# Optimization experiments

Hardware: AMD Instinct MI355X
Metric: run time of the kernel (lower is better)

Reference implementation:

```python
import jax, jax.numpy as jnp
import numpy as np

N = 100000      # nodes
E = 1600000     # edges
D_IN = 16       # input_dim
D_H = 32        # hidden_dim
D_OUT = 1       # output_dim
N_ITERS = 2
D_CAT = D_H + D_IN          # node feature after cat([H, X])
D_EDGE = 2 * D_CAT          # edge MLP input dim


def setup_inputs() -> dict:
    key = jax.random.key(0)
    ks = jax.random.split(key, 10)
    x = jax.random.normal(ks[0], (N, D_IN), jnp.float32)
    edge_index = jax.random.randint(ks[1], (2, E), 0, N, dtype=jnp.int32)
    # inputnet: Linear(D_IN -> D_H) + Tanh
    W_in = jax.random.normal(ks[2], (D_H, D_IN), jnp.float32) / np.sqrt(D_IN)
    b_in = jnp.zeros((D_H,), jnp.float32)
    # convnn (EdgeConv nn): Linear(D_EDGE -> D_H) + Sigmoid
    W_c = jax.random.normal(ks[3], (D_H, D_EDGE), jnp.float32) / np.sqrt(D_EDGE)
    b_c = jnp.zeros((D_H,), jnp.float32)
    # outputnet: Linear(D_H -> D_OUT) + Sigmoid
    W_out = jax.random.normal(ks[4], (D_OUT, D_H), jnp.float32) / np.sqrt(D_H)
    b_out = jnp.zeros((D_OUT,), jnp.float32)
    return {"x": x, "edge_index": edge_index, "W_in": W_in, "b_in": b_in,
            "W_c": W_c, "b_c": b_c, "W_out": W_out, "b_out": b_out}


def reference(x, edge_index, W_in, b_in, W_c, b_c, W_out, b_out):
    src = edge_index[0]  # x_j (source / neighbor)
    dst = edge_index[1]  # x_i (target, aggregation index)

    H = jnp.tanh(x @ W_in.T + b_in)            # [N, D_H]
    feats = jnp.concatenate([H, x], axis=-1)    # [N, D_CAT]

    for _ in range(N_ITERS):
        xi = feats[dst]                          # [E, D_CAT] gather targets
        xj = feats[src]                          # [E, D_CAT] gather sources
        # PyG EdgeConv message: nn(cat([x_i, x_j - x_i]))
        msg = jax.nn.sigmoid(
            jnp.concatenate([xi, xj - xi], axis=-1) @ W_c.T + b_c)  # [E, D_H]
        H = jax.ops.segment_sum(msg, dst, num_segments=N)           # aggr='add'
        feats = jnp.concatenate([H, x], axis=-1)

    sum_H = jnp.mean(H, axis=0)                  # [D_H]
    return jax.nn.sigmoid(sum_H @ W_out.T + b_out)  # [D_OUT]
```

## Files before the change

kernel.cpp:

```cpp
#include <hip/hip_runtime.h>

#define D_H 32
#define NREP 32
#define SLOTS 48
#define BIN_SHIFT 8
#define MAXNB 512
#define BIN_CAP 5120
#define SB 256
#define PNPB 64
#define SF 52

__device__ __forceinline__ float sigf(float v) {
    return 1.f / (1.f + __expf(-v));
}


__global__ __launch_bounds__(256) void k_ab0(const float* __restrict__ x,
                      const float* __restrict__ W_in, const float* __restrict__ b_in,
                      const float* __restrict__ W_c, const float* __restrict__ b_c,
                      float* __restrict__ A, float* __restrict__ B, int N) {
    __shared__ float f[PNPB][SF];
    int tid = threadIdx.x;
    int n0 = blockIdx.x * PNPB;
    int wv = tid >> 6;
    int h  = (tid >> 5) & 1;
    int j  = tid & 31;
    float wc[96];
    {
        const float4* wr = (const float4*)(W_c + j * 96);
#pragma unroll
        for (int q = 0; q < 24; ++q) {
            float4 v = wr[q];
            wc[4 * q] = v.x; wc[4 * q + 1] = v.y; wc[4 * q + 2] = v.z; wc[4 * q + 3] = v.w;
        }
    }
    float win[16];
    {
        const float4* wr = (const float4*)(W_in + j * 16);
#pragma unroll
        for (int q = 0; q < 4; ++q) {
            float4 v = wr[q];
            win[4 * q] = v.x; win[4 * q + 1] = v.y; win[4 * q + 2] = v.z; win[4 * q + 3] = v.w;
        }
    }
    float bc = b_c[j];
    float bi = b_in[j];
    {
        int row = tid >> 2, c = tid & 3;
        float4 v = {0.f, 0.f, 0.f, 0.f};
        if (n0 + row < N) v = ((const float4*)(x + (size_t)(n0 + row) * 16))[c];
        *(float4*)&f[row][32 + 4 * c] = v;
    }
    __syncthreads();
#pragma unroll 2
    for (int it = 0; it < 8; ++it) {
        int n = wv * 16 + it * 2 + h;
        {
            float4 x0 = *(const float4*)&f[n][32];
            float4 x1 = *(const float4*)&f[n][36];
            float4 x2 = *(const float4*)&f[n][40];
            float4 x3 = *(const float4*)&f[n][44];
            float acc = bi;
            acc += x0.x * win[0] + x0.y * win[1] + x0.z * win[2] + x0.w * win[3];
            acc += x1.x * win[4] + x1.y * win[5] + x1.z * win[6] + x1.w * win[7];
            acc += x2.x * win[8] + x2.y * win[9] + x2.z * win[10] + x2.w * win[11];
            acc += x3.x * win[12] + x3.y * win[13] + x3.z * win[14] + x3.w * win[15];
            f[n][j] = tanhf(acc);
        }
        float p = bc, bb = 0.f;
#pragma unroll
        for (int q = 0; q < 12; ++q) {
            float4 v = *(const float4*)&f[n][4 * q];
            p  += v.x * wc[4 * q]      + v.y * wc[4 * q + 1]
                + v.z * wc[4 * q + 2]  + v.w * wc[4 * q + 3];
            bb += v.x * wc[48 + 4 * q]     + v.y * wc[48 + 4 * q + 1]
                + v.z * wc[48 + 4 * q + 2] + v.w * wc[48 + 4 * q + 3];
        }
        int g = n0 + n;
        if (g < N) {
            A[(size_t)g * D_H + j] = p - bb;
            B[(size_t)g * D_H + j] = bb;
        }
    }
}

__global__ __launch_bounds__(256) void k_ab1(const float* __restrict__ H,
                      const float* __restrict__ x, const float* __restrict__ W_c,
                      const float* __restrict__ b_c, float* __restrict__ A,
                      float* __restrict__ B, int N) {
    __shared__ float f[PNPB][SF];
    int tid = threadIdx.x;
    int n0 = blockIdx.x * PNPB;
    int wv = tid >> 6;
    int h  = (tid >> 5) & 1;
    int j  = tid & 31;
    float wc[96];
    {
        const float4* wr = (const float4*)(W_c + j * 96);
#pragma unroll
        for (int q = 0; q < 24; ++q) {
            float4 v = wr[q];
            wc[4 * q] = v.x; wc[4 * q + 1] = v.y; wc[4 * q + 2] = v.z; wc[4 * q + 3] = v.w;
        }
    }
    float bc = b_c[j];
#pragma unroll
    for (int k = 0; k < 2; ++k) {
        int i = k * 256 + tid;
        int row = i >> 3, c = i & 7;
        float4 v = {0.f, 0.f, 0.f, 0.f};
        if (n0 + row < N) v = ((const float4*)(H + (size_t)(n0 + row) * D_H))[c];
        *(float4*)&f[row][4 * c] = v;
    }
    {
        int row = tid >> 2, c = tid & 3;
        float4 v = {0.f, 0.f, 0.f, 0.f};
        if (n0 + row < N) v = ((const float4*)(x + (size_t)(n0 + row) * 16))[c];
        *(float4*)&f[row][32 + 4 * c] = v;
    }
    __syncthreads();
#pragma unroll 2
    for (int it = 0; it < 8; ++it) {
        int n = wv * 16 + it * 2 + h;
        float p = bc, bb = 0.f;
#pragma unroll
        for (int q = 0; q < 12; ++q) {
            float4 v = *(const float4*)&f[n][4 * q];
            p  += v.x * wc[4 * q]      + v.y * wc[4 * q + 1]
                + v.z * wc[4 * q + 2]  + v.w * wc[4 * q + 3];
            bb += v.x * wc[48 + 4 * q]     + v.y * wc[48 + 4 * q + 1]
                + v.z * wc[48 + 4 * q + 2] + v.w * wc[48 + 4 * q + 3];
        }
        int g = n0 + n;
        if (g < N) {
            A[(size_t)g * D_H + j] = p - bb;
            B[(size_t)g * D_H + j] = bb;
        }
    }
}

__global__ __launch_bounds__(256) void k_bin(const int* __restrict__ src,
                                             const int* __restrict__ dst,
                                             int* __restrict__ binCnt,
                                             unsigned int* __restrict__ ebuf, int E) {
    __shared__ int hist[MAXNB];
    int tid = threadIdx.x;
    for (int i = tid; i < MAXNB; i += 256) hist[i] = 0;
    __syncthreads();
    int chunk = (E + SB - 1) / SB;
    int lo = blockIdx.x * chunk;
    int hi = lo + chunk; if (hi > E) hi = E;
    for (int e = lo + tid; e < hi; e += 256) {
        int b = dst[e] >> BIN_SHIFT;
        atomicAdd(&hist[b], 1);
    }
    __syncthreads();
    for (int b = tid; b < MAXNB; b += 256) {
        int c = hist[b];
        int base = c ? atomicAdd(&binCnt[b], c) : 0;
        hist[b] = b * BIN_CAP + base;
    }
    __syncthreads();
    for (int e = lo + tid; e < hi; e += 256) {
        int d = dst[e];
        int s = src[e];
        int b = d >> BIN_SHIFT;
        int pos = atomicAdd(&hist[b], 1);
        if ((unsigned)(pos - b * BIN_CAP) < (unsigned)BIN_CAP)
            ebuf[pos] = ((unsigned)(d & 255) << 24) | (unsigned)s;
    }
}

__global__ __launch_bounds__(256) void k_place(const int* __restrict__ binCnt,
                                               const unsigned int* __restrict__ ebuf,
                                               int* __restrict__ ssrcp,
                                               int* __restrict__ cntG,
                                               float* __restrict__ Srep, int N) {
    __shared__ int cnt[256];
    int tid = threadIdx.x;
    int w = blockIdx.x;
    if (w == 0) {
        float4 z = {0.f, 0.f, 0.f, 0.f};
        ((float4*)Srep)[tid];
        ((float4*)Srep)[tid] = z;
    }
    cnt[tid] = 0;
    __syncthreads();
    int n = binCnt[w]; if (n > BIN_CAP) n = BIN_CAP;
    int base = w * BIN_CAP;
    for (int j = tid; j < n; j += 256) {
        unsigned int v = ebuf[base + j];
        int ld = v >> 24;
        int s = v & 0xFFFFFF;
        int slot = atomicAdd(&cnt[ld], 1);
        if (slot < SLOTS)
            ssrcp[(size_t)((w << BIN_SHIFT) + ld) * SLOTS + slot] = s;
    }
    __syncthreads();
    int node = (w << BIN_SHIFT) + tid;
    if (node < N) cntG[node] = cnt[tid] < SLOTS ? cnt[tid] : SLOTS;
}


__global__ __launch_bounds__(256) void k_gather1(const int* __restrict__ cntG,
                          const int* __restrict__ ssrcp,
                          const float* __restrict__ A, const float* __restrict__ B,
                          float* __restrict__ H, int N) {
    int t = blockIdx.x * blockDim.x + threadIdx.x;
    int d = t >> 5;
    if (d >= N) return;
    int l = t & 31;
    int q = l & 7;
    int s = l >> 3;
    int len = cntG[d];
    const int* base = ssrcp + (size_t)d * SLOTS;
    float4 a4 = ((const float4*)(A + (size_t)d * D_H))[q];
    float4 acc = {0.f, 0.f, 0.f, 0.f};
    int j = s;
    for (; j + 12 < len; j += 16) {
        int i0 = base[j], i1 = base[j + 4], i2 = base[j + 8], i3 = base[j + 12];
        float4 b0 = ((const float4*)(B + (size_t)i0 * D_H))[q];
        float4 b1 = ((const float4*)(B + (size_t)i1 * D_H))[q];
        float4 b2 = ((const float4*)(B + (size_t)i2 * D_H))[q];
        float4 b3 = ((const float4*)(B + (size_t)i3 * D_H))[q];
        acc.x += sigf(a4.x + b0.x); acc.y += sigf(a4.y + b0.y);
        acc.z += sigf(a4.z + b0.z); acc.w += sigf(a4.w + b0.w);
        acc.x += sigf(a4.x + b1.x); acc.y += sigf(a4.y + b1.y);
        acc.z += sigf(a4.z + b1.z); acc.w += sigf(a4.w + b1.w);
        acc.x += sigf(a4.x + b2.x); acc.y += sigf(a4.y + b2.y);
        acc.z += sigf(a4.z + b2.z); acc.w += sigf(a4.w + b2.w);
        acc.x += sigf(a4.x + b3.x); acc.y += sigf(a4.y + b3.y);
        acc.z += sigf(a4.z + b3.z); acc.w += sigf(a4.w + b3.w);
    }
    for (; j + 4 < len; j += 8) {
        int i0 = base[j], i1 = base[j + 4];
        float4 b0 = ((const float4*)(B + (size_t)i0 * D_H))[q];
        float4 b1 = ((const float4*)(B + (size_t)i1 * D_H))[q];
        acc.x += sigf(a4.x + b0.x); acc.y += sigf(a4.y + b0.y);
        acc.z += sigf(a4.z + b0.z); acc.w += sigf(a4.w + b0.w);
        acc.x += sigf(a4.x + b1.x); acc.y += sigf(a4.y + b1.y);
        acc.z += sigf(a4.z + b1.z); acc.w += sigf(a4.w + b1.w);
    }
    if (j < len) {
        int i0 = base[j];
        float4 b0 = ((const float4*)(B + (size_t)i0 * D_H))[q];
        acc.x += sigf(a4.x + b0.x); acc.y += sigf(a4.y + b0.y);
        acc.z += sigf(a4.z + b0.z); acc.w += sigf(a4.w + b0.w);
    }
    acc.x += __shfl_xor(acc.x, 8);  acc.y += __shfl_xor(acc.y, 8);
    acc.z += __shfl_xor(acc.z, 8);  acc.w += __shfl_xor(acc.w, 8);
    acc.x += __shfl_xor(acc.x, 16); acc.y += __shfl_xor(acc.y, 16);
    acc.z += __shfl_xor(acc.z, 16); acc.w += __shfl_xor(acc.w, 16);
    if (s == 0) ((float4*)(H + (size_t)d * D_H))[q] = acc;
}

__global__ __launch_bounds__(256) void k_gather2(const int* __restrict__ cntG,
                          const int* __restrict__ ssrcp,
                          const float* __restrict__ A, const float* __restrict__ B,
                          float* __restrict__ Srep, int N) {
    int l = threadIdx.x & 31;
    int slot = threadIdx.x >> 5;
    int q = l & 7;
    int s = l >> 3;
    int d = blockIdx.x * 8 + slot;
    float4 acc = {0.f, 0.f, 0.f, 0.f};
    if (d < N) {
        int len = cntG[d];
        const int* base = ssrcp + (size_t)d * SLOTS;
        float4 a4 = ((const float4*)(A + (size_t)d * D_H))[q];
        int j = s;
        for (; j + 12 < len; j += 16) {
            int i0 = base[j], i1 = base[j + 4], i2 = base[j + 8], i3 = base[j + 12];
            float4 b0 = ((const float4*)(B + (size_t)i0 * D_H))[q];
            float4 b1 = ((const float4*)(B + (size_t)i1 * D_H))[q];
            float4 b2 = ((const float4*)(B + (size_t)i2 * D_H))[q];
            float4 b3 = ((const float4*)(B + (size_t)i3 * D_H))[q];
            acc.x += sigf(a4.x + b0.x); acc.y += sigf(a4.y + b0.y);
            acc.z += sigf(a4.z + b0.z); acc.w += sigf(a4.w + b0.w);
            acc.x += sigf(a4.x + b1.x); acc.y += sigf(a4.y + b1.y);
            acc.z += sigf(a4.z + b1.z); acc.w += sigf(a4.w + b1.w);
            acc.x += sigf(a4.x + b2.x); acc.y += sigf(a4.y + b2.y);
            acc.z += sigf(a4.z + b2.z); acc.w += sigf(a4.w + b2.w);
            acc.x += sigf(a4.x + b3.x); acc.y += sigf(a4.y + b3.y);
            acc.z += sigf(a4.z + b3.z); acc.w += sigf(a4.w + b3.w);
        }
        for (; j + 4 < len; j += 8) {
            int i0 = base[j], i1 = base[j + 4];
            float4 b0 = ((const float4*)(B + (size_t)i0 * D_H))[q];
            float4 b1 = ((const float4*)(B + (size_t)i1 * D_H))[q];
            acc.x += sigf(a4.x + b0.x); acc.y += sigf(a4.y + b0.y);
            acc.z += sigf(a4.z + b0.z); acc.w += sigf(a4.w + b0.w);
            acc.x += sigf(a4.x + b1.x); acc.y += sigf(a4.y + b1.y);
            acc.z += sigf(a4.z + b1.z); acc.w += sigf(a4.w + b1.w);
        }
        if (j < len) {
            int i0 = base[j];
            float4 b0 = ((const float4*)(B + (size_t)i0 * D_H))[q];
            acc.x += sigf(a4.x + b0.x); acc.y += sigf(a4.y + b0.y);
            acc.z += sigf(a4.z + b0.z); acc.w += sigf(a4.w + b0.w);
        }
    }
    acc.x += __shfl_xor(acc.x, 8);  acc.y += __shfl_xor(acc.y, 8);
    acc.z += __shfl_xor(acc.z, 8);  acc.w += __shfl_xor(acc.w, 8);
    acc.x += __shfl_xor(acc.x, 16); acc.y += __shfl_xor(acc.y, 16);
    acc.z += __shfl_xor(acc.z, 16); acc.w += __shfl_xor(acc.w, 16);
    __shared__ float red[8][32];
    if (s == 0) {
        red[slot][4 * q + 0] = acc.x;
        red[slot][4 * q + 1] = acc.y;
        red[slot][4 * q + 2] = acc.z;
        red[slot][4 * q + 3] = acc.w;
    }
    __syncthreads();
    if (threadIdx.x < 32) {
        float sm = 0.f;
#pragma unroll
        for (int r = 0; r < 8; ++r) sm += red[r][threadIdx.x];
        unsafeAtomicAdd(&Srep[(blockIdx.x & (NREP - 1)) * D_H + threadIdx.x], sm);
    }
}

__global__ void k_final(const float* __restrict__ Srep, const float* __restrict__ W_out,
                        const float* __restrict__ b_out, float* __restrict__ out,
                        float invN) {
    int j = threadIdx.x;
    float v = 0.f;
    if (j < 32) {
        float s = 0.f;
#pragma unroll
        for (int r = 0; r < NREP; ++r) s += Srep[r * D_H + j];
        v = s * invN * W_out[j];
    }
#pragma unroll
    for (int off = 32; off > 0; off >>= 1) v += __shfl_down(v, off);
    if (j == 0) out[0] = 1.f / (1.f + __expf(-(v + b_out[0])));
}

extern "C" void kernel_launch(void* const* d_in, const int* in_sizes, int n_in,
                              void* d_out, int out_size, void* d_ws, size_t ws_size,
                              hipStream_t stream) {
    const float* x     = (const float*)d_in[0];
    const int*   ei    = (const int*)d_in[1];
    const float* W_in  = (const float*)d_in[2];
    const float* b_in  = (const float*)d_in[3];
    const float* W_c   = (const float*)d_in[4];
    const float* b_c   = (const float*)d_in[5];
    const float* W_out = (const float*)d_in[6];
    const float* b_out = (const float*)d_in[7];

    const int N = in_sizes[0] / 16;
    const int E = in_sizes[1] / 2;
    const int* src = ei;
    const int* dst = ei + E;

    const int NB = (N + 255) >> BIN_SHIFT;

    float* H    = (float*)d_ws;
    float* A    = H + (size_t)N * D_H;
    float* B    = A + (size_t)N * D_H;
    float* Srep = B + (size_t)N * D_H;
    int*   cntG   = (int*)(Srep + NREP * D_H);
    int*   binCnt = cntG + N;
    int*   ssrcp  = binCnt + MAXNB;
    unsigned int* ebuf = (unsigned int*)H;

    float* out = (float*)d_out;

    const int abBlocks = (N + PNPB - 1) / PNPB;

    hipMemsetAsync(binCnt, 0, MAXNB * sizeof(int), stream);
    k_bin<<<SB, 256, 0, stream>>>(src, dst, binCnt, ebuf, E);
    k_place<<<NB, 256, 0, stream>>>(binCnt, ebuf, ssrcp, cntG, Srep, N);

    k_ab0<<<abBlocks, 256, 0, stream>>>(x, W_in, b_in, W_c, b_c, A, B, N);
    k_gather1<<<(int)(((size_t)N * 32 + 255) / 256), 256, 0, stream>>>(cntG, ssrcp, A, B, H, N);

    k_ab1<<<abBlocks, 256, 0, stream>>>(H, x, W_c, b_c, A, B, N);
    k_gather2<<<(N + 7) / 8, 256, 0, stream>>>(cntG, ssrcp, A, B, Srep, N);

    k_final<<<1, 64, 0, stream>>>(Srep, W_out, b_out, out, 1.f / (float)N);
}
```

Before: 267.4 us.

## Store gathered B in fp16, fold log2e scaling, vectorize neighbor index loads

The per-source B table is now stored as half precision and pre-scaled by -log2(e), and A is pre-scaled the same way. The gather loops can then compute the sigmoid with exp2 plus a hardware reciprocal, and each random neighbor fetch moves 8 bytes instead of 16. Neighbor lists are padded with zeros to a multiple of four so each lane can read four indices with one int4 load, with padded entries masked out by a multiplier. This cuts random-gather bandwidth and per-edge ALU work at the cost of fp16 rounding error in the message inputs.

```diff
diff --git a/kernel.cpp b/kernel.cpp
--- a/kernel.cpp
+++ b/kernel.cpp
@@ -1,4 +1,5 @@
 #include <hip/hip_runtime.h>
+#include <hip/hip_fp16.h>
 
 #define D_H 32
 #define NREP 32
@@ -9,16 +10,13 @@
 #define SB 256
 #define PNPB 64
 #define SF 52
-
-__device__ __forceinline__ float sigf(float v) {
-    return 1.f / (1.f + __expf(-v));
-}
+#define L2E 1.4426950408889634f
 
 
 __global__ __launch_bounds__(256) void k_ab0(const float* __restrict__ x,
                       const float* __restrict__ W_in, const float* __restrict__ b_in,
                       const float* __restrict__ W_c, const float* __restrict__ b_c,
-                      float* __restrict__ A, float* __restrict__ B, int N) {
+                      float* __restrict__ A, __half* __restrict__ Bh, int N) {
     __shared__ float f[PNPB][SF];
     int tid = threadIdx.x;
     int n0 = blockIdx.x * PNPB;
@@ -78,8 +76,8 @@
         }
         int g = n0 + n;
         if (g < N) {
-            A[(size_t)g * D_H + j] = p - bb;
-            B[(size_t)g * D_H + j] = bb;
+            A[(size_t)g * D_H + j]  = -L2E * (p - bb);
+            Bh[(size_t)g * D_H + j] = __float2half_rn(-L2E * bb);
         }
     }
 }
@@ -87,7 +85,7 @@
 __global__ __launch_bounds__(256) void k_ab1(const float* __restrict__ H,
                       const float* __restrict__ x, const float* __restrict__ W_c,
                       const float* __restrict__ b_c, float* __restrict__ A,
-                      float* __restrict__ B, int N) {
+                      __half* __restrict__ Bh, int N) {
     __shared__ float f[PNPB][SF];
     int tid = threadIdx.x;
     int n0 = blockIdx.x * PNPB;
@@ -133,8 +131,8 @@
         }
         int g = n0 + n;
         if (g < N) {
-            A[(size_t)g * D_H + j] = p - bb;
-            B[(size_t)g * D_H + j] = bb;
+            A[(size_t)g * D_H + j]  = -L2E * (p - bb);
+            Bh[(size_t)g * D_H + j] = __float2half_rn(-L2E * bb);
         }
     }
 }
@@ -181,7 +179,6 @@
     int w = blockIdx.x;
     if (w == 0) {
         float4 z = {0.f, 0.f, 0.f, 0.f};
-        ((float4*)Srep)[tid];
         ((float4*)Srep)[tid] = z;
     }
     cnt[tid] = 0;
@@ -198,13 +195,19 @@
     }
     __syncthreads();
     int node = (w << BIN_SHIFT) + tid;
-    if (node < N) cntG[node] = cnt[tid] < SLOTS ? cnt[tid] : SLOTS;
+    if (node < N) {
+        int c = cnt[tid] < SLOTS ? cnt[tid] : SLOTS;
+        cntG[node] = c;
+        int cp = (c + 3) & ~3;
+        for (int t2 = c; t2 < cp; ++t2)
+            ssrcp[(size_t)node * SLOTS + t2] = 0;
+    }
 }
 
 
 __global__ __launch_bounds__(256) void k_gather1(const int* __restrict__ cntG,
                           const int* __restrict__ ssrcp,
-                          const float* __restrict__ A, const float* __restrict__ B,
+                          const float* __restrict__ A, const __half* __restrict__ Bh,
                           float* __restrict__ H, int N) {
     int t = blockIdx.x * blockDim.x + threadIdx.x;
     int d = t >> 5;
@@ -216,36 +219,30 @@
     const int* base = ssrcp + (size_t)d * SLOTS;
     float4 a4 = ((const float4*)(A + (size_t)d * D_H))[q];
     float4 acc = {0.f, 0.f, 0.f, 0.f};
-    int j = s;
-    for (; j + 12 < len; j += 16) {
-        int i0 = base[j], i1 = base[j + 4], i2 = base[j + 8], i3 = base[j + 12];
-        float4 b0 = ((const float4*)(B + (size_t)i0 * D_H))[q];
-        float4 b1 = ((const float4*)(B + (size_t)i1 * D_H))[q];
-        float4 b2 = ((const float4*)(B + (size_t)i2 * D_H))[q];
-        float4 b3 = ((const float4*)(B + (size_t)i3 * D_H))[q];
-        acc.x += sigf(a4.x + b0.x); acc.y += sigf(a4.y + b0.y);
-        acc.z += sigf(a4.z + b0.z); acc.w += sigf(a4.w + b0.w);
-        acc.x += sigf(a4.x + b1.x); acc.y += sigf(a4.y + b1.y);
-        acc.z += sigf(a4.z + b1.z); acc.w += sigf(a4.w + b1.w);
-        acc.x += sigf(a4.x + b2.x); acc.y += sigf(a4.y + b2.y);
-        acc.z += sigf(a4.z + b2.z); acc.w += sigf(a4.w + b2.w);
-        acc.x += sigf(a4.x + b3.x); acc.y += sigf(a4.y + b3.y);
-        acc.z += sigf(a4.z + b3.z); acc.w += sigf(a4.w + b3.w);
-    }
-    for (; j + 4 < len; j += 8) {
-        int i0 = base[j], i1 = base[j + 4];
-        float4 b0 = ((const float4*)(B + (size_t)i0 * D_H))[q];
-        float4 b1 = ((const float4*)(B + (size_t)i1 * D_H))[q];
-        acc.x += sigf(a4.x + b0.x); acc.y += sigf(a4.y + b0.y);
-        acc.z += sigf(a4.z + b0.z); acc.w += sigf(a4.w + b0.w);
-        acc.x += sigf(a4.x + b1.x); acc.y += sigf(a4.y + b1.y);
-        acc.z += sigf(a4.z + b1.z); acc.w += sigf(a4.w + b1.w);
-    }
-    if (j < len) {
-        int i0 = base[j];
-        float4 b0 = ((const float4*)(B + (size_t)i0 * D_H))[q];
-        acc.x += sigf(a4.x + b0.x); acc.y += sigf(a4.y + b0.y);
-        acc.z += sigf(a4.z + b0.z); acc.w += sigf(a4.w + b0.w);
+    for (int bj = 0; bj < len; bj += 16) {
+        int jj = bj + 4 * s;
+        if (jj < len) {
+            int4 iv = *(const int4*)(base + jj);
+            int rem = len - jj;
+#pragma unroll
+            for (int k = 0; k < 4; ++k) {
+                int idx = ((const int*)&iv)[k];
+                float vld = (k < rem) ? 1.f : 0.f;
+                uint2 u = *(const uint2*)(Bh + (size_t)idx * D_H + 4 * q);
+                __half2 h0 = *reinterpret_cast<const __half2*>(&u.x);
+                __half2 h1 = *reinterpret_cast<const __half2*>(&u.y);
+                float2 f0 = __half22float2(h0);
+                float2 f1 = __half22float2(h1);
+                float e0 = exp2f(a4.x + f0.x);
+                float e1 = exp2f(a4.y + f0.y);
+                float e2 = exp2f(a4.z + f1.x);
+                float e3 = exp2f(a4.w + f1.y);
+                acc.x = fmaf(vld, __builtin_amdgcn_rcpf(1.f + e0), acc.x);
+                acc.y = fmaf(vld, __builtin_amdgcn_rcpf(1.f + e1), acc.y);
+                acc.z = fmaf(vld, __builtin_amdgcn_rcpf(1.f + e2), acc.z);
+                acc.w = fmaf(vld, __builtin_amdgcn_rcpf(1.f + e3), acc.w);
+            }
+        }
     }
     acc.x += __shfl_xor(acc.x, 8);  acc.y += __shfl_xor(acc.y, 8);
     acc.z += __shfl_xor(acc.z, 8);  acc.w += __shfl_xor(acc.w, 8);
@@ -256,7 +253,7 @@
 
 __global__ __launch_bounds__(256) void k_gather2(const int* __restrict__ cntG,
                           const int* __restrict__ ssrcp,
-                          const float* __restrict__ A, const float* __restrict__ B,
+                          const float* __restrict__ A, const __half* __restrict__ Bh,
                           float* __restrict__ Srep, int N) {
     int l = threadIdx.x & 31;
     int slot = threadIdx.x >> 5;
@@ -268,36 +265,30 @@
         int len = cntG[d];
         const int* base = ssrcp + (size_t)d * SLOTS;
         float4 a4 = ((const float4*)(A + (size_t)d * D_H))[q];
-        int j = s;
-        for (; j + 12 < len; j += 16) {
-            int i0 = base[j], i1 = base[j + 4], i2 = base[j + 8], i3 = base[j + 12];
-            float4 b0 = ((const float4*)(B + (size_t)i0 * D_H))[q];
-            float4 b1 = ((const float4*)(B + (size_t)i1 * D_H))[q];
-            float4 b2 = ((const float4*)(B + (size_t)i2 * D_H))[q];
-            float4 b3 = ((const float4*)(B + (size_t)i3 * D_H))[q];
-            acc.x += sigf(a4.x + b0.x); acc.y += sigf(a4.y + b0.y);
-            acc.z += sigf(a4.z + b0.z); acc.w += sigf(a4.w + b0.w);
-            acc.x += sigf(a4.x + b1.x); acc.y += sigf(a4.y + b1.y);
-            acc.z += sigf(a4.z + b1.z); acc.w += sigf(a4.w + b1.w);
-            acc.x += sigf(a4.x + b2.x); acc.y += sigf(a4.y + b2.y);
-            acc.z += sigf(a4.z + b2.z); acc.w += sigf(a4.w + b2.w);
-            acc.x += sigf(a4.x + b3.x); acc.y += sigf(a4.y + b3.y);
-            acc.z += sigf(a4.z + b3.z); acc.w += sigf(a4.w + b3.w);
-        }
-        for (; j + 4 < len; j += 8) {
-            int i0 = base[j], i1 = base[j + 4];
-            float4 b0 = ((const float4*)(B + (size_t)i0 * D_H))[q];
-            float4 b1 = ((const float4*)(B + (size_t)i1 * D_H))[q];
-            acc.x += sigf(a4.x + b0.x); acc.y += sigf(a4.y + b0.y);
-            acc.z += sigf(a4.z + b0.z); acc.w += sigf(a4.w + b0.w);
-            acc.x += sigf(a4.x + b1.x); acc.y += sigf(a4.y + b1.y);
-            acc.z += sigf(a4.z + b1.z); acc.w += sigf(a4.w + b1.w);
-        }
-        if (j < len) {
-            int i0 = base[j];
-            float4 b0 = ((const float4*)(B + (size_t)i0 * D_H))[q];
-            acc.x += sigf(a4.x + b0.x); acc.y += sigf(a4.y + b0.y);
-            acc.z += sigf(a4.z + b0.z); acc.w += sigf(a4.w + b0.w);
+        for (int bj = 0; bj < len; bj += 16) {
+            int jj = bj + 4 * s;
+            if (jj < len) {
+                int4 iv = *(const int4*)(base + jj);
+                int rem = len - jj;
+#pragma unroll
+                for (int k = 0; k < 4; ++k) {
+                    int idx = ((const int*)&iv)[k];
+                    float vld = (k < rem) ? 1.f : 0.f;
+                    uint2 u = *(const uint2*)(Bh + (size_t)idx * D_H + 4 * q);
+                    __half2 h0 = *reinterpret_cast<const __half2*>(&u.x);
+                    __half2 h1 = *reinterpret_cast<const __half2*>(&u.y);
+                    float2 f0 = __half22float2(h0);
+                    float2 f1 = __half22float2(h1);
+                    float e0 = exp2f(a4.x + f0.x);
+                    float e1 = exp2f(a4.y + f0.y);
+                    float e2 = exp2f(a4.z + f1.x);
+                    float e3 = exp2f(a4.w + f1.y);
+                    acc.x = fmaf(vld, __builtin_amdgcn_rcpf(1.f + e0), acc.x);
+                    acc.y = fmaf(vld, __builtin_amdgcn_rcpf(1.f + e1), acc.y);
+                    acc.z = fmaf(vld, __builtin_amdgcn_rcpf(1.f + e2), acc.z);
+                    acc.w = fmaf(vld, __builtin_amdgcn_rcpf(1.f + e3), acc.w);
+                }
+            }
         }
     }
     acc.x += __shfl_xor(acc.x, 8);  acc.y += __shfl_xor(acc.y, 8);
@@ -357,8 +348,9 @@
 
     float* H    = (float*)d_ws;
     float* A    = H + (size_t)N * D_H;
-    float* B    = A + (size_t)N * D_H;
-    float* Srep = B + (size_t)N * D_H;
+    float* Breg = A + (size_t)N * D_H;
+    __half* Bh  = (__half*)Breg;
+    float* Srep = Breg + (size_t)N * D_H;
     int*   cntG   = (int*)(Srep + NREP * D_H);
     int*   binCnt = cntG + N;
     int*   ssrcp  = binCnt + MAXNB;
@@ -372,11 +364,11 @@
     k_bin<<<SB, 256, 0, stream>>>(src, dst, binCnt, ebuf, E);
     k_place<<<NB, 256, 0, stream>>>(binCnt, ebuf, ssrcp, cntG, Srep, N);
 
-    k_ab0<<<abBlocks, 256, 0, stream>>>(x, W_in, b_in, W_c, b_c, A, B, N);
-    k_gather1<<<(int)(((size_t)N * 32 + 255) / 256), 256, 0, stream>>>(cntG, ssrcp, A, B, H, N);
-
-    k_ab1<<<abBlocks, 256, 0, stream>>>(H, x, W_c, b_c, A, B, N);
-    k_gather2<<<(N + 7) / 8, 256, 0, stream>>>(cntG, ssrcp, A, B, Srep, N);
+    k_ab0<<<abBlocks, 256, 0, stream>>>(x, W_in, b_in, W_c, b_c, A, Bh, N);
+    k_gather1<<<(int)(((size_t)N * 32 + 255) / 256), 256, 0, stream>>>(cntG, ssrcp, A, Bh, H, N);
+
+    k_ab1<<<abBlocks, 256, 0, stream>>>(H, x, W_c, b_c, A, Bh, N);
+    k_gather2<<<(N + 7) / 8, 256, 0, stream>>>(cntG, ssrcp, A, Bh, Srep, N);
 
     k_final<<<1, 64, 0, stream>>>(Srep, W_out, b_out, out, 1.f / (float)N);
 }
```

New measurement: 246.6 us. -7.8%, faster.
